# Optimization experiments

Hardware: AMD Instinct MI355X
Metric: run time of the kernel (lower is better)

## Reference

```python
import jax, jax.numpy as jnp
import numpy as np
from jax import lax

NUM_GROUP = 2048
GROUP_SIZE = 16


def setup_inputs() -> dict:
    key = jax.random.key(0)
    pcd = jax.random.normal(key, (4, 16384, 3), dtype=jnp.float32)
    return {"pcd": pcd}


def _fps(xyz, n_samples):
    # Furthest point sampling, matching CUDA FPS: start at index 0,
    # iteratively pick the point with max min-distance to the chosen set.
    B, N, _ = xyz.shape

    def step(carry, _):
        min_d, last = carry
        p = jnp.take_along_axis(xyz, last[:, None, None], axis=1)  # B,1,3
        d = jnp.sum((xyz - p) ** 2, axis=-1)                       # B,N
        min_d = jnp.minimum(min_d, d)
        nxt = jnp.argmax(min_d, axis=-1).astype(jnp.int32)         # B
        return (min_d, nxt), nxt

    first = jnp.zeros((B,), jnp.int32)
    init = (jnp.full((B, N), 1e10, xyz.dtype), first)
    _, rest = lax.scan(step, init, None, length=n_samples - 1)     # (n-1),B
    return jnp.concatenate([first[None, :], rest], axis=0).T       # B,n


def reference(pcd):
    xyz = pcd                                                      # channel==3 path
    B, N, _ = xyz.shape
    # centers via FPS + gather (N != num_group branch)
    fps_idx = _fps(xyz, NUM_GROUP)                                 # B,G
    center = jnp.take_along_axis(xyz, fps_idx[:, :, None], axis=1) # B,G,3
    # kNN of each center among all points (squared L2)
    d2 = (jnp.sum(center * center, -1)[:, :, None]
          - 2.0 * jnp.einsum('bgc,bnc->bgn', center, xyz)
          + jnp.sum(xyz * xyz, -1)[:, None, :])                    # B,G,N
    _, idx = lax.top_k(-d2, GROUP_SIZE)                            # B,G,M (nearest first)
    # gather neighborhoods per batch
    nbr = jax.vmap(lambda x, i: x[i])(xyz, idx)                    # B,G,M,3
    neighborhood = nbr - center[:, :, None, :]
    return neighborhood, center
```

## Files before the change

kernel.cpp:

```cpp
#include <hip/hip_runtime.h>
#include <math.h>


#pragma clang fp contract(off)

#define N_PTS 16384
#define N_GROUP 2048
#define GROUP_SIZE 16
#define FPS_THREADS 512
#define PPT (N_PTS / FPS_THREADS)
#define FPS_WAVES (FPS_THREADS / 64)
#define KNN_THREADS 256
#define KNN_WAVES (KNN_THREADS / 64)

__device__ __forceinline__ float fmul_sep(float a, float b) {
  float r = a * b;
  asm volatile("" : "+v"(r));
  return r;
}

__device__ __forceinline__ unsigned long long shfl_xor_u64(unsigned long long v, int off) {
  const unsigned int lo = __shfl_xor((unsigned int)v, off);
  const unsigned int hi = __shfl_xor((unsigned int)(v >> 32), off);
  return ((unsigned long long)hi << 32) | lo;
}

__global__ __launch_bounds__(FPS_THREADS)
__attribute__((amdgpu_waves_per_eu(2, 2)))
void fps_kernel(const float* __restrict__ pcd, float* __restrict__ center) {
#pragma clang fp contract(off)
  const int b = blockIdx.x;
  const int t = threadIdx.x;
  const int lane = t & 63;
  const int wid = t >> 6;
  const float* xyz = pcd + (size_t)b * N_PTS * 3;

  __shared__ float2 xy[N_PTS];
  __shared__ unsigned long long skey[2][FPS_WAVES];
  __shared__ float szw[2][FPS_WAVES];

  float z[PPT], md[PPT];
#pragma unroll
  for (int i = 0; i < PPT; ++i) {
    const int idx = i * FPS_THREADS + t;
    const float xv = xyz[idx * 3 + 0];
    const float yv = xyz[idx * 3 + 1];
    z[i] = xyz[idx * 3 + 2];
    xy[idx] = make_float2(xv, yv);
    md[i] = 1e10f;
  }
#pragma unroll
  for (int i = 0; i < PPT; ++i) asm("" : "+v"(z[i]));

  float px = xyz[0], py = xyz[1], pz = xyz[2];
  if (t == 0) {
    center[((size_t)b * N_GROUP) * 3 + 0] = px;
    center[((size_t)b * N_GROUP) * 3 + 1] = py;
    center[((size_t)b * N_GROUP) * 3 + 2] = pz;
  }
  __syncthreads();

  for (int it = 1; it < N_GROUP; ++it) {
    const int p = it & 1;
    float bv = -1.0f;
    int bi = 0;
    float bz = 0.0f;
#pragma unroll
    for (int i = 0; i < PPT; ++i) {
      const float2 q = xy[i * FPS_THREADS + t];
      const float dx = q.x - px;
      const float dy = q.y - py;
      const float dz = z[i] - pz;
      const float d = ((dx * dx) + (dy * dy)) + (dz * dz);
      const float m = fminf(md[i], d);
      md[i] = m;
      if (m > bv) { bv = m; bi = i * FPS_THREADS + t; bz = z[i]; }
    }
    unsigned long long key =
        ((unsigned long long)__float_as_uint(bv) << 32) |
        (unsigned int)(N_PTS - 1 - bi);

#pragma unroll
    for (int off = 32; off > 0; off >>= 1) {
      const unsigned long long ok = shfl_xor_u64(key, off);
      const float oz = __shfl_xor(bz, off);
      if (ok > key) { key = ok; bz = oz; }
    }
    if (lane == 0) { skey[p][wid] = key; szw[p][wid] = bz; }
    __syncthreads();
    unsigned long long bk = skey[p][0];
    int bj = 0;
#pragma unroll
    for (int j = 1; j < FPS_WAVES; ++j) {
      const unsigned long long kj = skey[p][j];
      if (kj > bk) { bk = kj; bj = j; }
    }
    const int kidx = N_PTS - 1 - (int)(unsigned int)(bk & 0xffffffffu);
    const float2 pq = xy[kidx];
    px = pq.x; py = pq.y; pz = szw[p][bj];
    if (t == 0) {
      center[((size_t)b * N_GROUP + it) * 3 + 0] = px;
      center[((size_t)b * N_GROUP + it) * 3 + 1] = py;
      center[((size_t)b * N_GROUP + it) * 3 + 2] = pz;
    }
  }
}

__global__ __launch_bounds__(KNN_THREADS) void knn_kernel(
    const float* __restrict__ pcd, const float* __restrict__ center,
    float* __restrict__ nbr) {
#pragma clang fp contract(off)
  const int lane = threadIdx.x & 63;
  const int gw = blockIdx.x * KNN_WAVES + (threadIdx.x >> 6);
  const int b = gw >> 11;
  const float* xyz = pcd + (size_t)b * N_PTS * 3;

  const float c0 = center[(size_t)gw * 3 + 0];
  const float c1 = center[(size_t)gw * 3 + 1];
  const float c2 = center[(size_t)gw * 3 + 2];
  const float cc = (fmul_sep(c0, c0) + fmul_sep(c1, c1)) + fmul_sep(c2, c2);

  float lval = INFINITY;
  int lidx = 0;
  float worst = INFINITY;

  for (int ch = 0; ch < N_PTS / 64; ++ch) {
    const int n = ch * 64 + lane;
    const float xp = xyz[n * 3 + 0];
    const float yp = xyz[n * 3 + 1];
    const float zp = xyz[n * 3 + 2];
    const float xx = (fmul_sep(xp, xp) + fmul_sep(yp, yp)) + fmul_sep(zp, zp);
    const float dot = fmaf(c2, zp, fmaf(c1, yp, c0 * xp));
    const float d2 = (cc - fmul_sep(2.0f, dot)) + xx;

    unsigned long long m = __ballot(d2 < worst);
    while (m) {
      const int srcl = __ffsll((unsigned long long)m) - 1;
      m &= (m - 1);
      const float nv = __shfl(d2, srcl);
      if (nv < worst) {
        const int ni = ch * 64 + srcl;
        const int rank = __popcll(__ballot(lane < GROUP_SIZE && lval <= nv));
        const float shv = __shfl_up(lval, 1);
        const int   shi = __shfl_up(lidx, 1);
        if (lane < GROUP_SIZE) {
          if (lane == rank)      { lval = nv;  lidx = ni;  }
          else if (lane > rank)  { lval = shv; lidx = shi; }
        }
        worst = __shfl(lval, 15);
      }
    }
  }

  if (lane < GROUP_SIZE) {
    const float ox = xyz[lidx * 3 + 0] - c0;
    const float oy = xyz[lidx * 3 + 1] - c1;
    const float oz = xyz[lidx * 3 + 2] - c2;
    const size_t o = ((size_t)gw * GROUP_SIZE + lane) * 3;
    nbr[o + 0] = ox; nbr[o + 1] = oy; nbr[o + 2] = oz;
  }
}

extern "C" void kernel_launch(void* const* d_in, const int* in_sizes, int n_in,
                              void* d_out, int out_size, void* d_ws, size_t ws_size,
                              hipStream_t stream) {
  const float* pcd = (const float*)d_in[0];
  const int B = in_sizes[0] / (N_PTS * 3);

  float* out = (float*)d_out;
  float* nbr = out;
  float* center = out + (size_t)B * N_GROUP * GROUP_SIZE * 3;

  fps_kernel<<<B, FPS_THREADS, 0, stream>>>(pcd, center);
  knn_kernel<<<(B * N_GROUP) / KNN_WAVES, KNN_THREADS, 0, stream>>>(pcd, center, nbr);
}
```

Baseline: 4.355 ms.

## Double FPS block to 1024 threads and reduce cross-wave winners in one wave

Doubles the FPS block to 1024 threads, which halves points per thread and raises waves per EU to 4. The per-thread argmax now tracks only the loop index. The final reduction over 16 wave winners moves from a serial per-thread scan to a shuffle reduction in wave 0, which broadcasts the chosen center through shared memory. This adds a second __syncthreads per iteration and more cross-wave reduction in exchange for more parallelism in the distance update. Only 4 blocks run, so most of the GPU stays idle either way.

```diff
diff --git a/kernel.cpp b/kernel.cpp
--- a/kernel.cpp
+++ b/kernel.cpp
@@ -7,7 +7,7 @@
 #define N_PTS 16384
 #define N_GROUP 2048
 #define GROUP_SIZE 16
-#define FPS_THREADS 512
+#define FPS_THREADS 1024
 #define PPT (N_PTS / FPS_THREADS)
 #define FPS_WAVES (FPS_THREADS / 64)
 #define KNN_THREADS 256
@@ -26,7 +26,7 @@
 }
 
 __global__ __launch_bounds__(FPS_THREADS)
-__attribute__((amdgpu_waves_per_eu(2, 2)))
+__attribute__((amdgpu_waves_per_eu(4, 4)))
 void fps_kernel(const float* __restrict__ pcd, float* __restrict__ center) {
 #pragma clang fp contract(off)
   const int b = blockIdx.x;
@@ -38,6 +38,7 @@
   __shared__ float2 xy[N_PTS];
   __shared__ unsigned long long skey[2][FPS_WAVES];
   __shared__ float szw[2][FPS_WAVES];
+  __shared__ float bcx[2], bcy[2], bcz[2];
 
   float z[PPT], md[PPT];
 #pragma unroll
@@ -63,7 +64,7 @@
   for (int it = 1; it < N_GROUP; ++it) {
     const int p = it & 1;
     float bv = -1.0f;
-    int bi = 0;
+    int ii = 0;
     float bz = 0.0f;
 #pragma unroll
     for (int i = 0; i < PPT; ++i) {
@@ -74,8 +75,9 @@
       const float d = ((dx * dx) + (dy * dy)) + (dz * dz);
       const float m = fminf(md[i], d);
       md[i] = m;
-      if (m > bv) { bv = m; bi = i * FPS_THREADS + t; bz = z[i]; }
+      if (m > bv) { bv = m; ii = i; bz = z[i]; }
     }
+    const int bi = ii * FPS_THREADS + t;
     unsigned long long key =
         ((unsigned long long)__float_as_uint(bv) << 32) |
         (unsigned int)(N_PTS - 1 - bi);
@@ -88,21 +90,27 @@
     }
     if (lane == 0) { skey[p][wid] = key; szw[p][wid] = bz; }
     __syncthreads();
-    unsigned long long bk = skey[p][0];
-    int bj = 0;
+
+    if (wid == 0) {
+      unsigned long long k = skey[p][lane & 15];
+      float zz = szw[p][lane & 15];
 #pragma unroll
-    for (int j = 1; j < FPS_WAVES; ++j) {
-      const unsigned long long kj = skey[p][j];
-      if (kj > bk) { bk = kj; bj = j; }
+      for (int off = 8; off > 0; off >>= 1) {
+        const unsigned long long ok = shfl_xor_u64(k, off);
+        const float oz = __shfl_xor(zz, off);
+        if (ok > k) { k = ok; zz = oz; }
+      }
+      if (lane == 0) {
+        const int kidx = N_PTS - 1 - (int)(unsigned int)(k & 0xffffffffu);
+        const float2 pq = xy[kidx];
+        bcx[p] = pq.x; bcy[p] = pq.y; bcz[p] = zz;
+        center[((size_t)b * N_GROUP + it) * 3 + 0] = pq.x;
+        center[((size_t)b * N_GROUP + it) * 3 + 1] = pq.y;
+        center[((size_t)b * N_GROUP + it) * 3 + 2] = zz;
+      }
     }
-    const int kidx = N_PTS - 1 - (int)(unsigned int)(bk & 0xffffffffu);
-    const float2 pq = xy[kidx];
-    px = pq.x; py = pq.y; pz = szw[p][bj];
-    if (t == 0) {
-      center[((size_t)b * N_GROUP + it) * 3 + 0] = px;
-      center[((size_t)b * N_GROUP + it) * 3 + 1] = py;
-      center[((size_t)b * N_GROUP + it) * 3 + 2] = pz;
-    }
+    __syncthreads();
+    px = bcx[p]; py = bcy[p]; pz = bcz[p];
   }
 }
 
```

Result: no change. 4.367 ms (+0.3%).
